# Kernel optimization log

Measured on AMD Instinct MI355X. Metric: run time of the kernel, lower is better.

## Reference

```python
import jax, jax.numpy as jnp
import numpy as np

B, T, D, H = 4, 2048, 1024, 16
DK = D // H


def setup_inputs() -> dict:
    key = jax.random.key(0)
    ks = jax.random.split(key, 9)
    s = 1.0 / np.sqrt(D)
    x = jax.random.normal(ks[0], (B, T, D), dtype=jnp.float32)
    mask = jnp.tril(jnp.ones((T, T), dtype=bool))[None, None]  # causal [1,1,T,T]
    wq = jax.random.uniform(ks[1], (D, D), jnp.float32, -s, s)
    bq = jax.random.uniform(ks[2], (D,), jnp.float32, -s, s)
    wk = jax.random.uniform(ks[3], (D, D), jnp.float32, -s, s)
    bk = jax.random.uniform(ks[4], (D,), jnp.float32, -s, s)
    wv = jax.random.uniform(ks[5], (D, D), jnp.float32, -s, s)
    bv = jax.random.uniform(ks[6], (D,), jnp.float32, -s, s)
    wo = jax.random.uniform(ks[7], (D, D), jnp.float32, -s, s)
    bo = jax.random.uniform(ks[8], (D,), jnp.float32, -s, s)
    return {"x": x, "mask": mask, "wq": wq, "bq": bq, "wk": wk, "bk": bk,
            "wv": wv, "bv": bv, "wo": wo, "bo": bo}


def reference(x, mask, wq, bq, wk, bk, wv, bv, wo, bo):
    # projections: torch Linear is x @ W.T + b; here weights stored as (D, D) used directly
    q = (x @ wq + bq).reshape(B, T, H, DK).transpose(0, 2, 1, 3)  # [B,H,T,dk]
    k = (x @ wk + bk).reshape(B, T, H, DK).transpose(0, 2, 1, 3)
    v = (x @ wv + bv).reshape(B, T, H, DK).transpose(0, 2, 1, 3)
    scores = jnp.einsum('bhqd,bhkd->bhqk', q, k) / jnp.sqrt(jnp.float32(DK))
    scores = jnp.where(mask, scores, -jnp.inf)
    attn = jax.nn.softmax(scores, axis=-1)
    # dropout p=0.0 -> identity
    y = jnp.einsum('bhqk,bhkd->bhqd', attn, v)
    y = y.transpose(0, 2, 1, 3).reshape(B, T, D)
    return y @ wo + bo
```

## Files before the change

### kernel.cpp

```cpp
#include <hip/hip_runtime.h>


typedef short s16x8 __attribute__((ext_vector_type(8)));
typedef short s16x4 __attribute__((ext_vector_type(4)));
typedef float f32x4 __attribute__((ext_vector_type(4)));
typedef unsigned int u32x2 __attribute__((ext_vector_type(2)));

static __device__ __forceinline__ float bf2f(unsigned short u) {
    return __uint_as_float(((unsigned int)u) << 16);
}
static __device__ __forceinline__ unsigned short f2bf(float f) {
    unsigned int x = __float_as_uint(f);
    unsigned int r = x + 0x7fffu + ((x >> 16) & 1u);
    return (unsigned short)(r >> 16);
}

static __device__ __forceinline__ void gload_lds16(const short* g, short* l) {
    __builtin_amdgcn_global_load_lds((__attribute__((address_space(1))) void*)g,
                                     (__attribute__((address_space(3))) void*)l, 16, 0, 0);
}

static __device__ __forceinline__ unsigned int cvt_pk_bf16(float a, float b) {
    unsigned int r;
    asm("v_cvt_pk_bf16_f32 %0, %1, %2" : "=v"(r) : "v"(a), "v"(b));
    return r;
}

static __device__ __forceinline__ float fexp2(float x) {
    float r;
    asm("v_exp_f32 %0, %1" : "=v"(r) : "v"(x));
    return r;
}

__global__ __launch_bounds__(64) void detect_dtype(const unsigned short* __restrict__ x,
                                                   int* __restrict__ flag) {
    int lane = threadIdx.x;
    int cnt = 0;
    for (int i = 0; i < 64; ++i) {
        float v = bf2f(x[lane * 64 + i]);
        if (!(fabsf(v) < 1e10f)) cnt++;
    }
    unsigned long long m = __ballot(cnt > 0);
    if (lane == 0) *flag = (m != 0ull) ? 1 : 0;
}

__global__ __launch_bounds__(256) void convert_bf16(const void* __restrict__ src,
                                                    unsigned short* __restrict__ dst,
                                                    int n, const int* __restrict__ flag) {
    int i = blockIdx.x * 256 + threadIdx.x;
    if (i >= n) return;
    if (*flag) dst[i] = f2bf(((const float*)src)[i]);
    else       dst[i] = ((const unsigned short*)src)[i];
}

__global__ __launch_bounds__(256) void convert_biases(const void* __restrict__ b0,
                                                      const void* __restrict__ b1,
                                                      const void* __restrict__ b2,
                                                      const void* __restrict__ b3,
                                                      unsigned short* __restrict__ dst,
                                                      const int* __restrict__ flag) {
    int i = blockIdx.x * 256 + threadIdx.x;
    const void* src = (i < 1024) ? b0 : (i < 2048 ? b1 : (i < 3072 ? b2 : b3));
    int k = i & 1023;
    if (*flag) dst[i] = f2bf(((const float*)src)[k]);
    else       dst[i] = ((const unsigned short*)src)[k];
}

__global__ __launch_bounds__(256) void transpose_wt(const void* __restrict__ src,
                                                    unsigned short* __restrict__ dst,
                                                    const int* __restrict__ flag) {
    __shared__ unsigned short t[32][33];
    int f = *flag;
    int x = threadIdx.x, y = threadIdx.y;
    int n0 = blockIdx.x * 32, k0 = blockIdx.y * 32;
    for (int j = 0; j < 32; j += 8) {
        size_t idx = (size_t)(k0 + y + j) * 1024 + n0 + x;
        t[y + j][x] = f ? f2bf(((const float*)src)[idx]) : ((const unsigned short*)src)[idx];
    }
    __syncthreads();
    for (int j = 0; j < 32; j += 8) dst[(size_t)(n0 + y + j) * 1024 + k0 + x] = t[x][y + j];
}

__global__ __launch_bounds__(256) void gemm_bf16(const short* __restrict__ A,
                                                 const short* __restrict__ Bt,
                                                 void* __restrict__ C,
                                                 short* __restrict__ vt,
                                                 const unsigned short* __restrict__ bq,
                                                 const unsigned short* __restrict__ bk,
                                                 const unsigned short* __restrict__ bv,
                                                 int K, int ldc,
                                                 const int* __restrict__ flag, int f32out,
                                                 int scale_q, int fuse_v) {
    __shared__ __align__(16) short As[128][64];
    __shared__ __align__(16) short Bs[128][64];
    int tid = threadIdx.x;
    int wid = tid >> 6, lane = tid & 63, quad = lane >> 4, l16 = lane & 15;
    int wm = wid & 1, wn = wid >> 1;
    int m0 = blockIdx.x * 128, n0 = blockIdx.y * 128;
    bool wf = f32out && (*flag != 0);

    int srow = lane >> 3;
    int schunk = (lane & 7) ^ srow;
    const short* Ag = A  + (size_t)(m0 + wid * 32 + srow) * K + schunk * 8;
    const short* Bg = Bt + (size_t)(n0 + wid * 32 + srow) * K + schunk * 8;
    short* Al = &As[wid * 32][0];
    short* Bl = &Bs[wid * 32][0];

    f32x4 acc[4][4] = {};
    for (int k0 = 0; k0 < K; k0 += 64) {
        __syncthreads();
#pragma unroll
        for (int c = 0; c < 4; ++c) {
            gload_lds16(Ag + k0 + c * 8 * K, Al + c * 512);
            gload_lds16(Bg + k0 + c * 8 * K, Bl + c * 512);
        }
        __syncthreads();
#pragma unroll
        for (int kk = 0; kk < 2; ++kk) {
            s16x8 a[4], b[4];
#pragma unroll
            for (int i = 0; i < 4; ++i) {
                int row = wm * 64 + i * 16 + l16;
                a[i] = *(const s16x8*)&As[row][(((kk << 2) + quad) ^ (row & 7)) << 3];
            }
#pragma unroll
            for (int j = 0; j < 4; ++j) {
                int row = wn * 64 + j * 16 + l16;
                b[j] = *(const s16x8*)&Bs[row][(((kk << 2) + quad) ^ (row & 7)) << 3];
            }
#pragma unroll
            for (int i = 0; i < 4; ++i)
#pragma unroll
                for (int j = 0; j < 4; ++j)
                    acc[i][j] = __builtin_amdgcn_mfma_f32_16x16x32_bf16(a[i], b[j], acc[i][j], 0, 0, 0);
        }
    }
    for (int j = 0; j < 4; ++j) {
        int col = n0 + wn * 64 + j * 16 + l16;
        const unsigned short* bptr = (col < 1024) ? bq : (col < 2048 ? bk : bv);
        float bias = bf2f(bptr[col & 1023]);
        float cs = (scale_q && col < 1024) ? 0.18033688f : 1.0f;
        for (int i = 0; i < 4; ++i) {
            int rbase = m0 + wm * 64 + i * 16 + quad * 4;
            if (fuse_v && col >= 2048) {
                int h = (col - 2048) >> 6, dk = col & 63;
                int bb_ = rbase >> 11, t = rbase & 2047;
                s16x4 pk;
                for (int r = 0; r < 4; ++r) pk[r] = (short)f2bf(acc[i][j][r] + bias);
                *(s16x4*)(vt + ((size_t)((bb_ * 16 + h) * 64 + dk)) * 2048 + t) = pk;
            } else {
                for (int r = 0; r < 4; ++r) {
                    float v = (acc[i][j][r] + bias) * cs;
                    size_t idx = (size_t)(rbase + r) * ldc + col;
                    if (wf) ((float*)C)[idx] = v;
                    else    ((unsigned short*)C)[idx] = f2bf(v);
                }
            }
        }
    }
}

static __device__ __forceinline__ void stage_tiles(const short* kbase, const short* vbase,
                                                   int kt, short* Kb, short* Vb,
                                                   int wid, int lane) {
    int row = wid * 8 + (lane >> 3);
    int c_src = (lane & 7) ^ (lane >> 3);
    const short* kg = kbase + (size_t)(kt * 64 + row) * 3072 + c_src * 8;
    const short* vg = vbase + (size_t)row * 2048 + kt * 64 + c_src * 8;
    gload_lds16(kg, Kb + wid * 512);
    gload_lds16(vg, Vb + wid * 512);
}

static __device__ __forceinline__ s16x8 lds_frag(const short* buf, int row, int cg) {
    int slot = cg ^ (row & 7);
    return *(const s16x8*)(buf + row * 64 + slot * 8);
}

__global__ __launch_bounds__(512, 4) void attn(const short* __restrict__ qkv,
                                               const short* __restrict__ vt,
                                               unsigned short* __restrict__ y) {
    __shared__ __align__(16) short Kbuf[3][64 * 64];
    __shared__ __align__(16) short Vbuf[3][64 * 64];
    __shared__ __align__(16) short Ps[8][16 * 68];
    int tid = threadIdx.x;
    int wid = tid >> 6, lane = tid & 63, quad = lane >> 4, l16 = lane & 15;
    int bh = blockIdx.x, b = bh >> 4, h = bh & 15;
    const short* kbase = qkv + (size_t)b * 2048 * 3072 + 1024 + h * 64;
    const short* vbase = vt + (size_t)bh * 64 * 2048;
    short* PsW = &Ps[wid][0];

    s16x8 ones;
    for (int e = 0; e < 8; ++e) ones[e] = (short)0x3F80;

    int qb = 15 - (int)blockIdx.y;
    int ktmax = 2 * qb + 1;
    int kmax_w = 2 * qb + (wid >> 2);

    const short* qp = qkv + (size_t)(b * 2048 + qb * 128 + wid * 16 + l16) * 3072 + h * 64;
    s16x8 q0 = *(const s16x8*)(qp + quad * 8);
    s16x8 q1 = *(const s16x8*)(qp + 32 + quad * 8);

    float m_old = -INFINITY;
    f32x4 lacc = {0.f, 0.f, 0.f, 0.f};
    f32x4 o[4] = {};

    stage_tiles(kbase, vbase, 0, &Kbuf[0][0], &Vbuf[0][0], wid, lane);
    stage_tiles(kbase, vbase, 1, &Kbuf[1][0], &Vbuf[1][0], wid, lane);
    int ss = 2;
    int cc = 0;

    for (int kt = 0; kt <= ktmax; ++kt) {
        if (kt < ktmax) asm volatile("s_waitcnt vmcnt(2)" ::: "memory");
        else            asm volatile("s_waitcnt vmcnt(0)" ::: "memory");
        __builtin_amdgcn_sched_barrier(0);
        __builtin_amdgcn_s_barrier();

        if (kt + 2 <= ktmax) {
            stage_tiles(kbase, vbase, kt + 2, &Kbuf[0][0] + ss * 4096, &Vbuf[0][0] + ss * 4096,
                        wid, lane);
            ss = (ss == 2) ? 0 : ss + 1;
        }

        if (kt <= kmax_w) {
            const short* Kb = &Kbuf[0][0] + cc * 4096;
            const short* Vb = &Vbuf[0][0] + cc * 4096;

            f32x4 s[4] = {};
            __builtin_amdgcn_s_setprio(1);
            for (int j = 0; j < 4; ++j) {
                s16x8 klo = lds_frag(Kb, j * 16 + l16, quad);
                s16x8 khi = lds_frag(Kb, j * 16 + l16, 4 + quad);
                s[j] = __builtin_amdgcn_mfma_f32_16x16x32_bf16(klo, q0, s[j], 0, 0, 0);
                s[j] = __builtin_amdgcn_mfma_f32_16x16x32_bf16(khi, q1, s[j], 0, 0, 0);
            }
            __builtin_amdgcn_s_setprio(0);

            if (kt == kmax_w) {
                int qq = (wid & 3) * 16 + l16;
                for (int j = 0; j < 4; ++j)
                    for (int r = 0; r < 4; ++r)
                        if (j * 16 + quad * 4 + r > qq) s[j][r] = -INFINITY;
            }

            float mj0 = fmaxf(fmaxf(s[0][0], s[0][1]), s[0][2]);
            mj0 = fmaxf(mj0, s[0][3]);
            float mj1 = fmaxf(fmaxf(s[1][0], s[1][1]), s[1][2]);
            mj1 = fmaxf(mj1, s[1][3]);
            float mj2 = fmaxf(fmaxf(s[2][0], s[2][1]), s[2][2]);
            mj2 = fmaxf(mj2, s[2][3]);
            float mj3 = fmaxf(fmaxf(s[3][0], s[3][1]), s[3][2]);
            mj3 = fmaxf(mj3, s[3][3]);
            float mx = fmaxf(fmaxf(fmaxf(mj0, mj1), mj2), mj3);
            mx = fmaxf(mx, __shfl_xor(mx, 16));
            mx = fmaxf(mx, __shfl_xor(mx, 32));

            if (__any(mx > m_old + 8.0f)) {
                float mn = fmaxf(m_old, mx);
                float alpha = fexp2(m_old - mn);
                m_old = mn;
                float ar[4];
                for (int r = 0; r < 4; ++r) ar[r] = __shfl(alpha, quad * 4 + r);
                for (int r = 0; r < 4; ++r) {
                    lacc[r] *= ar[r];
                    for (int d = 0; d < 4; ++d) o[d][r] *= ar[r];
                }
            }

            for (int j = 0; j < 4; ++j) {
                float p0 = fexp2(s[j][0] - m_old);
                float p1 = fexp2(s[j][1] - m_old);
                float p2 = fexp2(s[j][2] - m_old);
                float p3 = fexp2(s[j][3] - m_old);
                u32x2 w;
                w.x = cvt_pk_bf16(p0, p1);
                w.y = cvt_pk_bf16(p2, p3);
                *(u32x2*)(PsW + l16 * 68 + j * 16 + quad * 4) = w;
            }

            s16x8 pa0 = *(const s16x8*)&PsW[l16 * 68 + quad * 8];
            s16x8 pa1 = *(const s16x8*)&PsW[l16 * 68 + 32 + quad * 8];
            __builtin_amdgcn_s_setprio(1);
            lacc = __builtin_amdgcn_mfma_f32_16x16x32_bf16(pa0, ones, lacc, 0, 0, 0);
            lacc = __builtin_amdgcn_mfma_f32_16x16x32_bf16(pa1, ones, lacc, 0, 0, 0);
            for (int d = 0; d < 4; ++d) {
                s16x8 vlo = lds_frag(Vb, d * 16 + l16, quad);
                s16x8 vhi = lds_frag(Vb, d * 16 + l16, 4 + quad);
                o[d] = __builtin_amdgcn_mfma_f32_16x16x32_bf16(pa0, vlo, o[d], 0, 0, 0);
                o[d] = __builtin_amdgcn_mfma_f32_16x16x32_bf16(pa1, vhi, o[d], 0, 0, 0);
            }
            __builtin_amdgcn_s_setprio(0);
        }
        cc = (cc == 2) ? 0 : cc + 1;
    }

    for (int r = 0; r < 4; ++r) {
        float inv = 1.f / lacc[r];
        int t = qb * 128 + wid * 16 + quad * 4 + r;
        for (int d = 0; d < 4; ++d)
            y[(size_t)(b * 2048 + t) * 1024 + h * 64 + d * 16 + l16] = f2bf(o[d][r] * inv);
    }
}

extern "C" void kernel_launch(void* const* d_in, const int* in_sizes, int n_in,
                              void* d_out, int out_size, void* d_ws, size_t ws_size,
                              hipStream_t stream) {
    (void)in_sizes; (void)n_in; (void)out_size; (void)ws_size;
    const void* x  = d_in[0];
    const void* wq = d_in[2]; const void* bq = d_in[3];
    const void* wk = d_in[4]; const void* bk = d_in[5];
    const void* wv = d_in[6]; const void* bv = d_in[7];
    const void* wo = d_in[8]; const void* bo = d_in[9];

    const size_t MB = 1024 * 1024;
    char* ws = (char*)d_ws;
    unsigned short* wT  = (unsigned short*)ws;
    short* qkv = (short*)(ws + 8 * MB);
    short* vt  = (short*)(ws + 56 * MB);
    unsigned short* xb = (unsigned short*)(ws + 72 * MB);
    unsigned short* yb = (unsigned short*)(ws + 72 * MB);
    unsigned short* bb = (unsigned short*)(ws + 88 * MB);
    int* flag = (int*)(ws + 88 * MB + 64 * 1024);

    detect_dtype<<<1, 64, 0, stream>>>((const unsigned short*)x, flag);
    convert_bf16<<<32768, 256, 0, stream>>>(x, xb, 8388608, flag);
    convert_biases<<<16, 256, 0, stream>>>(bq, bk, bv, bo, bb, flag);

    dim3 tb(32, 8);
    transpose_wt<<<dim3(32, 32), tb, 0, stream>>>(wq, wT,                flag);
    transpose_wt<<<dim3(32, 32), tb, 0, stream>>>(wk, wT + 1024 * 1024,  flag);
    transpose_wt<<<dim3(32, 32), tb, 0, stream>>>(wv, wT + 2048 * 1024,  flag);
    transpose_wt<<<dim3(32, 32), tb, 0, stream>>>(wo, wT + 3072 * 1024,  flag);

    gemm_bf16<<<dim3(64, 24), 256, 0, stream>>>((const short*)xb, (const short*)wT,
                                                qkv, vt, bb, bb + 1024, bb + 2048,
                                                1024, 3072, flag, 0, 1, 1);
    attn<<<dim3(64, 16), 512, 0, stream>>>(qkv, vt, yb);
    gemm_bf16<<<dim3(64, 8), 256, 0, stream>>>((const short*)yb, (const short*)(wT + 3072 * 1024),
                                               d_out, nullptr, bb + 3072, bb + 3072, bb + 3072,
                                               1024, 1024, flag, 1, 0, 0);
}
```

Measured before the change: 316.6 us.

## Double-buffer GEMM LDS tiles and merge weight transposes into one launch

The GEMM now keeps two LDS buffers for the A and B tiles, so the global-to-LDS load of the next k-tile is issued while the MFMAs run on the current one, with one barrier per iteration instead of two. It also raises wave priority around the MFMA block. The four weight-transpose launches are merged into a single launch that uses blockIdx.z to pick the matrix, which removes launch overhead. Doubling LDS to 64KB per block may reduce occupancy. Without a wait on the async load before the barrier, the prefetch correctness relies on the barrier draining vmcnt.

```diff
diff --git a/kernel.cpp b/kernel.cpp
--- a/kernel.cpp
+++ b/kernel.cpp
@@ -66,10 +66,16 @@
     else       dst[i] = ((const unsigned short*)src)[k];
 }
 
-__global__ __launch_bounds__(256) void transpose_wt(const void* __restrict__ src,
-                                                    unsigned short* __restrict__ dst,
-                                                    const int* __restrict__ flag) {
+__global__ __launch_bounds__(256) void transpose_wt4(const void* __restrict__ s0,
+                                                     const void* __restrict__ s1,
+                                                     const void* __restrict__ s2,
+                                                     const void* __restrict__ s3,
+                                                     unsigned short* __restrict__ dst,
+                                                     const int* __restrict__ flag) {
     __shared__ unsigned short t[32][33];
+    int z = blockIdx.z;
+    const void* src = (z == 0) ? s0 : (z == 1 ? s1 : (z == 2 ? s2 : s3));
+    dst += (size_t)z * 1024 * 1024;
     int f = *flag;
     int x = threadIdx.x, y = threadIdx.y;
     int n0 = blockIdx.x * 32, k0 = blockIdx.y * 32;
@@ -91,8 +97,8 @@
                                                  int K, int ldc,
                                                  const int* __restrict__ flag, int f32out,
                                                  int scale_q, int fuse_v) {
-    __shared__ __align__(16) short As[128][64];
-    __shared__ __align__(16) short Bs[128][64];
+    __shared__ __align__(16) short As[2][128][64];
+    __shared__ __align__(16) short Bs[2][128][64];
     int tid = threadIdx.x;
     int wid = tid >> 6, lane = tid & 63, quad = lane >> 4, l16 = lane & 15;
     int wm = wid & 1, wn = wid >> 1;
@@ -103,37 +109,50 @@
     int schunk = (lane & 7) ^ srow;
     const short* Ag = A  + (size_t)(m0 + wid * 32 + srow) * K + schunk * 8;
     const short* Bg = Bt + (size_t)(n0 + wid * 32 + srow) * K + schunk * 8;
-    short* Al = &As[wid * 32][0];
-    short* Bl = &Bs[wid * 32][0];
 
     f32x4 acc[4][4] = {};
-    for (int k0 = 0; k0 < K; k0 += 64) {
-        __syncthreads();
-#pragma unroll
-        for (int c = 0; c < 4; ++c) {
-            gload_lds16(Ag + k0 + c * 8 * K, Al + c * 512);
-            gload_lds16(Bg + k0 + c * 8 * K, Bl + c * 512);
-        }
-        __syncthreads();
+    int nt = K >> 6;
+
+#pragma unroll
+    for (int c = 0; c < 4; ++c) {
+        gload_lds16(Ag + c * 8 * K, &As[0][wid * 32 + c * 8][0]);
+        gload_lds16(Bg + c * 8 * K, &Bs[0][wid * 32 + c * 8][0]);
+    }
+    __syncthreads();
+
+    for (int t = 0; t < nt; ++t) {
+        if (t + 1 < nt) {
+            int bu = (t + 1) & 1;
+            int kof = (t + 1) * 64;
+#pragma unroll
+            for (int c = 0; c < 4; ++c) {
+                gload_lds16(Ag + kof + c * 8 * K, &As[bu][wid * 32 + c * 8][0]);
+                gload_lds16(Bg + kof + c * 8 * K, &Bs[bu][wid * 32 + c * 8][0]);
+            }
+        }
+        const short (*Ab)[64] = As[t & 1];
 #pragma unroll
         for (int kk = 0; kk < 2; ++kk) {
             s16x8 a[4], b[4];
 #pragma unroll
             for (int i = 0; i < 4; ++i) {
                 int row = wm * 64 + i * 16 + l16;
-                a[i] = *(const s16x8*)&As[row][(((kk << 2) + quad) ^ (row & 7)) << 3];
+                a[i] = *(const s16x8*)&Ab[row][(((kk << 2) + quad) ^ (row & 7)) << 3];
             }
 #pragma unroll
             for (int j = 0; j < 4; ++j) {
                 int row = wn * 64 + j * 16 + l16;
-                b[j] = *(const s16x8*)&Bs[row][(((kk << 2) + quad) ^ (row & 7)) << 3];
-            }
+                b[j] = *(const s16x8*)&Bs[t & 1][row][(((kk << 2) + quad) ^ (row & 7)) << 3];
+            }
+            __builtin_amdgcn_s_setprio(1);
 #pragma unroll
             for (int i = 0; i < 4; ++i)
 #pragma unroll
                 for (int j = 0; j < 4; ++j)
                     acc[i][j] = __builtin_amdgcn_mfma_f32_16x16x32_bf16(a[i], b[j], acc[i][j], 0, 0, 0);
-        }
+            __builtin_amdgcn_s_setprio(0);
+        }
+        __syncthreads();
     }
     for (int j = 0; j < 4; ++j) {
         int col = n0 + wn * 64 + j * 16 + l16;
@@ -326,10 +345,7 @@
     convert_biases<<<16, 256, 0, stream>>>(bq, bk, bv, bo, bb, flag);
 
     dim3 tb(32, 8);
-    transpose_wt<<<dim3(32, 32), tb, 0, stream>>>(wq, wT,                flag);
-    transpose_wt<<<dim3(32, 32), tb, 0, stream>>>(wk, wT + 1024 * 1024,  flag);
-    transpose_wt<<<dim3(32, 32), tb, 0, stream>>>(wv, wT + 2048 * 1024,  flag);
-    transpose_wt<<<dim3(32, 32), tb, 0, stream>>>(wo, wT + 3072 * 1024,  flag);
+    transpose_wt4<<<dim3(32, 32, 4), tb, 0, stream>>>(wq, wk, wv, wo, wT, flag);
 
     gemm_bf16<<<dim3(64, 24), 256, 0, stream>>>((const short*)xb, (const short*)wT,
                                                 qkv, vt, bb, bb + 1024, bb + 2048,
```

New measurement: 299.7 us. 1.06x faster.
